# Performance work log

Hardware: AMD Instinct MI355X
Metric: run time of the kernel (lower is better)

## Reference

```python
import jax, jax.numpy as jnp
import numpy as np

HEADS = 16
DIM_HEAD = 64
RMS_EPS = 1.1920929e-07  # torch.finfo(float32).eps (torch RMSNorm eps=None default)
ROPE_THETA = 10000.0


def _rope(x):
    # x: [b, h, n, d]; rotary-embedding-torch style interleaved rotation
    n, d = x.shape[-2], x.shape[-1]
    inv_freq = 1.0 / (ROPE_THETA ** (jnp.arange(0, d, 2, dtype=jnp.float32) / d))
    t = jnp.arange(n, dtype=jnp.float32)
    freqs = t[:, None] * inv_freq[None, :]              # [n, d/2]
    cos = jnp.repeat(jnp.cos(freqs), 2, axis=-1)        # [n, d] interleaved
    sin = jnp.repeat(jnp.sin(freqs), 2, axis=-1)
    x1 = x[..., ::2]
    x2 = x[..., 1::2]
    rot = jnp.stack((-x2, x1), axis=-1).reshape(x.shape)  # rotate_half, interleaved pairs
    return x * cos + rot * sin


def setup_inputs() -> dict:
    key = jax.random.key(0)
    ks = jax.random.split(key, 6)
    b, n, dim = 2, 2048, 1024
    tokens = jax.random.normal(ks[0], (b, n, dim), dtype=jnp.float32)
    norm_weight = jnp.ones((dim,), dtype=jnp.float32)
    wq = jax.random.normal(ks[1], (dim, dim), dtype=jnp.float32) * 0.02
    wk = jax.random.normal(ks[2], (dim, dim), dtype=jnp.float32) * 0.02
    wv = jax.random.normal(ks[3], (dim, dim), dtype=jnp.float32) * 0.02
    wo = jax.random.normal(ks[4], (dim, dim), dtype=jnp.float32) * 0.02
    return {"tokens": tokens, "norm_weight": norm_weight, "wq": wq, "wk": wk, "wv": wv, "wo": wo}


def reference(tokens, norm_weight, wq, wk, wv, wo):
    b, n, dim = tokens.shape
    # RMSNorm (elementwise affine)
    x = tokens * jax.lax.rsqrt(jnp.mean(tokens * tokens, axis=-1, keepdims=True) + RMS_EPS)
    x = x * norm_weight
    # QKV projections (torch Linear: x @ W.T), split heads: b n (h d) -> b h n d
    def split(y):
        return y.reshape(b, n, HEADS, DIM_HEAD).transpose(0, 2, 1, 3)
    q = split(x @ wq.T) * (DIM_HEAD ** -0.5)
    k = split(x @ wk.T)
    v = split(x @ wv.T)
    # rotary embedding (no kv cache -> same positions for q and k)
    q = _rope(q)
    k = _rope(k)
    sim = jnp.einsum('bhid,bhjd->bhij', q, k)
    causal = jnp.triu(jnp.ones((n, n), dtype=bool), k=1)
    sim = jnp.where(causal, -jnp.finfo(sim.dtype).max, sim)
    attn = jax.nn.softmax(sim, axis=-1)
    out = jnp.einsum('bhij,bhjd->bhid', attn, v)
    out = out.transpose(0, 2, 1, 3).reshape(b, n, dim)  # merge heads
    return out @ wo.T
```

## Files before the change

### kernel.cpp

```cpp
#include <hip/hip_runtime.h>

typedef __bf16 bf16x8 __attribute__((ext_vector_type(8)));
typedef float f32x4 __attribute__((ext_vector_type(4)));

#define DIM 1024
#define NSEQ 2048

#define GL2LDS(g, l) __builtin_amdgcn_global_load_lds( \
    (const __attribute__((address_space(1))) void*)(g), \
    (__attribute__((address_space(3))) void*)(l), 16, 0, 0)

#define MFMA16(a, b, c) __builtin_amdgcn_mfma_f32_16x16x32_bf16(a, b, c, 0, 0, 0)

__global__ __launch_bounds__(256) void pre_kernel(const float* __restrict__ wq,
                                                  const float* __restrict__ wk,
                                                  const float* __restrict__ wv,
                                                  __bf16* __restrict__ dq,
                                                  __bf16* __restrict__ dk,
                                                  __bf16* __restrict__ dv,
                                                  float2* __restrict__ tbl,
                                                  int* __restrict__ counters,
                                                  const float* __restrict__ x,
                                                  const float* __restrict__ g,
                                                  __bf16* __restrict__ xo) {
    int bid = blockIdx.x;
    int t = threadIdx.x;
    if (bid == 0 && t < 8) counters[t] = 0;
    if (bid < 3072) {
        int slice = bid >> 10;
        const float* s = slice == 0 ? wq : (slice == 1 ? wk : wv);
        __bf16*      d = slice == 0 ? dq : (slice == 1 ? dk : dv);
        int i = ((bid & 1023) * 256 + t) * 4;
        float4 f = *(const float4*)(s + i);
        union { uint2 u; __bf16 h[4]; } p;
        p.h[0] = (__bf16)f.x; p.h[1] = (__bf16)f.y;
        p.h[2] = (__bf16)f.z; p.h[3] = (__bf16)f.w;
        *(uint2*)(d + i) = p.u;
    } else if (bid < 3328) {
        int e = (bid - 3072) * 256 + t;
        int pos = e >> 5, dp = e & 31;
        float inv = __expf(-(float)dp * (9.210340371976184f / 32.0f));
        float sn, cs;
        sincosf((float)pos * inv, &sn, &cs);
        tbl[e] = make_float2(cs, sn);
    } else {
        int row = bid - 3328;
        float4 xv = ((const float4*)(x + (size_t)row * DIM))[t];
        float ss = xv.x*xv.x + xv.y*xv.y + xv.z*xv.z + xv.w*xv.w;
        #pragma unroll
        for (int off = 32; off; off >>= 1) ss += __shfl_xor(ss, off, 64);
        __shared__ float red[4];
        if ((t & 63) == 0) red[t >> 6] = ss;
        __syncthreads();
        ss = red[0] + red[1] + red[2] + red[3];
        float r = rsqrtf(ss * (1.0f / 1024.0f) + 1.1920929e-07f);
        float4 gv = ((const float4*)g)[t];
        union { uint2 u; __bf16 h[4]; } p;
        p.h[0] = (__bf16)(xv.x * r * gv.x);
        p.h[1] = (__bf16)(xv.y * r * gv.y);
        p.h[2] = (__bf16)(xv.z * r * gv.z);
        p.h[3] = (__bf16)(xv.w * r * gv.w);
        *(uint2*)(xo + (size_t)row * DIM + t * 4) = p.u;
    }
}

template <typename CT, bool ROPE>
__device__ __forceinline__ void gemm_body(const __bf16* __restrict__ A,
                                          const __bf16* __restrict__ B,
                                          CT* __restrict__ C,
                                          int mb, int nb, int ldc, float scale,
                                          __bf16* As, __bf16* Bs,
                                          const float2* __restrict__ tbl) {
    int t = threadIdx.x;
    int w = t >> 6, l = t & 63;
    int wm = (w >> 1) * 64, wn = (w & 1) * 64;
    int lrow = l & 15, lq = l >> 4;
    int sw = lrow & 7;
    f32x4 acc[4][4] = {};

    int srow = w * 32 + (l >> 3);
    int sc8 = ((l & 7) ^ ((l >> 3) & 7)) * 8;
    const __bf16* gA = A + (size_t)(mb * 128 + srow) * 1024 + sc8;
    const __bf16* gB = B + (size_t)(nb * 128 + srow) * 1024 + sc8;
    __bf16* lA = As + (size_t)(w * 32) * 64;
    __bf16* lB = Bs + (size_t)(w * 32) * 64;

    for (int kt = 0; kt < 16; ++kt) {
        int k0 = kt * 64;
        #pragma unroll
        for (int c = 0; c < 4; ++c) {
            GL2LDS(gA + (size_t)c * 8 * 1024 + k0, lA + c * 8 * 64);
            GL2LDS(gB + (size_t)c * 8 * 1024 + k0, lB + c * 8 * 64);
        }
        __syncthreads();
        #pragma unroll
        for (int ch = 0; ch < 2; ++ch) {
            bf16x8 af[4], bfr[4];
            #pragma unroll
            for (int i = 0; i < 4; ++i)
                af[i] = *(const bf16x8*)&As[(wm + i * 16 + lrow) * 64 + ((ch * 4 + lq) ^ sw) * 8];
            #pragma unroll
            for (int i = 0; i < 4; ++i)
                bfr[i] = *(const bf16x8*)&Bs[(wn + i * 16 + lrow) * 64 + ((ch * 4 + lq) ^ sw) * 8];
            #pragma unroll
            for (int rt = 0; rt < 4; ++rt)
                #pragma unroll
                for (int ct = 0; ct < 4; ++ct)
                    acc[rt][ct] = MFMA16(af[rt], bfr[ct], acc[rt][ct]);
        }
        __syncthreads();
    }
    #pragma unroll
    for (int rt = 0; rt < 4; ++rt)
        #pragma unroll
        for (int ct = 0; ct < 4; ++ct) {
            int colg = nb * 128 + wn + ct * 16 + lrow;
            int dp = ((ct * 16 + lrow) & 63) >> 1;
            #pragma unroll
            for (int r = 0; r < 4; ++r) {
                int rowg = mb * 128 + wm + rt * 16 + lq * 4 + r;
                float v = acc[rt][ct][r] * scale;
                if constexpr (ROPE) {
                    float p = __shfl_xor(v, 1, 64);
                    float2 cs = tbl[((rowg & (NSEQ - 1)) << 5) + dp];
                    v = (lrow & 1) ? (v * cs.x + p * cs.y)
                                   : (v * cs.x - p * cs.y);
                }
                C[(size_t)rowg * ldc + colg] = (CT)v;
            }
        }
}

__global__ __launch_bounds__(256) void qkv_kernel(const __bf16* __restrict__ x,
                                                  const __bf16* __restrict__ wq,
                                                  const __bf16* __restrict__ wk,
                                                  const __bf16* __restrict__ wv,
                                                  __bf16* __restrict__ qb,
                                                  __bf16* __restrict__ kb,
                                                  __bf16* __restrict__ vtb,
                                                  const float2* __restrict__ tbl) {
    __shared__ __bf16 As[128 * 64];
    __shared__ __bf16 Bs[128 * 64];
    int bm = blockIdx.x, bn = blockIdx.y, z = blockIdx.z;
    if (z == 0)      gemm_body<__bf16, true >(x,  wq, qb,  bm, bn, 1024,
                                       0.125f * 1.44269504088896340736f, As, Bs, tbl);
    else if (z == 1) gemm_body<__bf16, true >(x,  wk, kb,  bm, bn, 1024, 1.0f, As, Bs, tbl);
    else             gemm_body<__bf16, false>(wv, x,  vtb, bn, bm, 4096, 1.0f, As, Bs, tbl);
}

__global__ __launch_bounds__(256) void wo_kernel(const __bf16* __restrict__ A,
                                                 const float* __restrict__ B,
                                                 float* __restrict__ C) {
    __shared__ __bf16 As[128 * 64];
    __shared__ __bf16 Bs[64 * 64];
    int mb = blockIdx.x, nb = blockIdx.y;
    int t = threadIdx.x;
    int w = t >> 6, l = t & 63;
    int wm = (w >> 1) * 64, wn = (w & 1) * 32;
    int lrow = l & 15, lq = l >> 4;
    int sw = lrow & 7;
    f32x4 acc[4][2] = {};

    int srowA = w * 32 + (l >> 3);
    int sc8 = ((l & 7) ^ ((l >> 3) & 7)) * 8;
    const __bf16* gA = A + (size_t)(mb * 128 + srowA) * 1024 + sc8;
    __bf16* lA = As + (size_t)(w * 32) * 64;

    int rB = t >> 2;
    const float* gB = B + (size_t)(nb * 64 + rB) * 1024 + (t & 3) * 16;
    int db0 = (rB * 8 + (((t & 3) * 2    ) ^ (rB & 7))) * 8;
    int db1 = (rB * 8 + (((t & 3) * 2 + 1) ^ (rB & 7))) * 8;

    for (int kt = 0; kt < 16; ++kt) {
        int k0 = kt * 64;
        #pragma unroll
        for (int c = 0; c < 4; ++c)
            GL2LDS(gA + (size_t)c * 8 * 1024 + k0, lA + c * 8 * 64);
        float4 b0 = *(const float4*)(gB + k0);
        float4 b1 = *(const float4*)(gB + k0 + 4);
        float4 b2 = *(const float4*)(gB + k0 + 8);
        float4 b3 = *(const float4*)(gB + k0 + 12);
        union { uint4 u; __bf16 h[8]; } p0, p1;
        p0.h[0] = (__bf16)b0.x; p0.h[1] = (__bf16)b0.y;
        p0.h[2] = (__bf16)b0.z; p0.h[3] = (__bf16)b0.w;
        p0.h[4] = (__bf16)b1.x; p0.h[5] = (__bf16)b1.y;
        p0.h[6] = (__bf16)b1.z; p0.h[7] = (__bf16)b1.w;
        p1.h[0] = (__bf16)b2.x; p1.h[1] = (__bf16)b2.y;
        p1.h[2] = (__bf16)b2.z; p1.h[3] = (__bf16)b2.w;
        p1.h[4] = (__bf16)b3.x; p1.h[5] = (__bf16)b3.y;
        p1.h[6] = (__bf16)b3.z; p1.h[7] = (__bf16)b3.w;
        *(uint4*)&Bs[db0] = p0.u;
        *(uint4*)&Bs[db1] = p1.u;
        __syncthreads();
        #pragma unroll
        for (int ch = 0; ch < 2; ++ch) {
            bf16x8 af[4], bfr[2];
            #pragma unroll
            for (int i = 0; i < 4; ++i)
                af[i] = *(const bf16x8*)&As[(wm + i * 16 + lrow) * 64 + ((ch * 4 + lq) ^ sw) * 8];
            #pragma unroll
            for (int i = 0; i < 2; ++i)
                bfr[i] = *(const bf16x8*)&Bs[(wn + i * 16 + lrow) * 64 + ((ch * 4 + lq) ^ sw) * 8];
            #pragma unroll
            for (int rt = 0; rt < 4; ++rt)
                #pragma unroll
                for (int ct = 0; ct < 2; ++ct)
                    acc[rt][ct] = MFMA16(af[rt], bfr[ct], acc[rt][ct]);
        }
        __syncthreads();
    }
    #pragma unroll
    for (int rt = 0; rt < 4; ++rt)
        #pragma unroll
        for (int ct = 0; ct < 2; ++ct)
            #pragma unroll
            for (int r = 0; r < 4; ++r) {
                int row = mb * 128 + wm + rt * 16 + lq * 4 + r;
                int col = nb * 64 + wn + ct * 16 + lrow;
                C[(size_t)row * 1024 + col] = acc[rt][ct][r];
            }
}

__global__ __launch_bounds__(256, 3) void attn_kernel(const __bf16* __restrict__ q,
                                                      const __bf16* __restrict__ kk,
                                                      const __bf16* __restrict__ vt,
                                                      __bf16* __restrict__ o,
                                                      int* __restrict__ counters) {
    int xcd = blockIdx.x & 7;
    int t = threadIdx.x;
    int w = t >> 6, l = t & 63;
    int lrow = l & 15, lq = l >> 4;
    int rw = (w & 1) * 32;
    int par = w >> 1;
    int row0 = t >> 3;
    int cb = t & 7;

    __shared__ __bf16 Kt[2][64 * 64];
    __shared__ __bf16 Vs[2][64 * 64];
    __shared__ __bf16 Ps[4][32 * 72];
    __shared__ int s_item;
    __bf16* pw = Ps[w];

    int dsw0 = (row0 * 8 + (cb ^ (row0 & 7))) * 8;
    int dsw1 = ((row0 + 32) * 8 + (cb ^ (row0 & 7))) * 8;

    if (t == 0) s_item = atomicAdd(&counters[xcd], 1);
    __syncthreads();
    int item = s_item;
    bool pf_valid = false;
    uint4 k0a, k0b, v0a, v0b, k1a, k1b, v1a, v1b;

    while (item < 128) {
        int iq = 31 - (item >> 2);
        int bh = xcd * 4 + (item & 3);
        int h = bh & 15;
        int b = bh >> 4;
        int rowbase = b * NSEQ;

        const __bf16* kbase = kk + (size_t)rowbase * DIM + h * 64;
        const __bf16* vbase = vt + (size_t)(h * 64) * 4096 + b * 2048;
        const __bf16* kg = kbase + (size_t)row0 * DIM + cb * 8;
        const __bf16* vg = vbase + (size_t)row0 * 4096 + cb * 8;

        bf16x8 qf[2][2];
        #pragma unroll
        for (int g = 0; g < 2; ++g) {
            const __bf16* qp = q + (size_t)(rowbase + iq * 64 + rw + g * 16 + lrow) * DIM + h * 64;
            qf[g][0] = *(const bf16x8*)(qp + lq * 8);
            qf[g][1] = *(const bf16x8*)(qp + 32 + lq * 8);
        }

        f32x4 oacc[2][4] = {};
        float m_r[2] = {-1e30f, -1e30f};
        float l_r[2] = {0.0f, 0.0f};

        if (!pf_valid) {
            k0a = *(const uint4*)(kg);
            k0b = *(const uint4*)(kg + (size_t)32 * DIM);
            v0a = *(const uint4*)(vg);
            v0b = *(const uint4*)(vg + (size_t)32 * 4096);
            if (iq >= 1) {
                k1a = *(const uint4*)(kg + (size_t)64 * DIM);
                k1b = *(const uint4*)(kg + (size_t)96 * DIM);
                v1a = *(const uint4*)(vg + 64);
                v1b = *(const uint4*)(vg + (size_t)32 * 4096 + 64);
            }
        }
        *(uint4*)&Kt[0][dsw0] = k0a; *(uint4*)&Kt[0][dsw1] = k0b;
        *(uint4*)&Vs[0][dsw0] = v0a; *(uint4*)&Vs[0][dsw1] = v0b;
        if (iq >= 1) {
            *(uint4*)&Kt[1][dsw0] = k1a; *(uint4*)&Kt[1][dsw1] = k1b;
            *(uint4*)&Vs[1][dsw0] = v1a; *(uint4*)&Vs[1][dsw1] = v1b;
        }
        __syncthreads();

        int R = (iq + 2) >> 1;
        for (int rd = 0; rd < R; ++rd) {
            if (rd == R - 1 && t == 0)
                s_item = atomicAdd(&counters[xcd], 1);
            int jt = 2 * rd + par;
            bool pf = (rd + 1 < R);
            if (pf) {
                int je = 2 * rd + 2;
                size_t ko = (size_t)je * 64 * DIM;
                k0a = *(const uint4*)(kg + ko);
                k0b = *(const uint4*)(kg + ko + (size_t)32 * DIM);
                v0a = *(const uint4*)(vg + je * 64);
                v0b = *(const uint4*)(vg + (size_t)32 * 4096 + je * 64);
                if (je + 1 <= iq) {
                    k1a = *(const uint4*)(kg + ko + (size_t)64 * DIM);
                    k1b = *(const uint4*)(kg + ko + (size_t)96 * DIM);
                    v1a = *(const uint4*)(vg + je * 64 + 64);
                    v1b = *(const uint4*)(vg + (size_t)32 * 4096 + je * 64 + 64);
                }
            }
            if (jt <= iq) {
                const __bf16* Kb = Kt[par];
                const __bf16* Vb = Vs[par];
                int sw = lrow & 7;
                f32x4 st[2][4];
                __builtin_amdgcn_s_setprio(1);
                #pragma unroll
                for (int ct = 0; ct < 4; ++ct) {
                    int rr = (ct * 16 + lrow) * 8;
                    bf16x8 ka0 = *(const bf16x8*)&Kb[(rr + (lq ^ sw)) * 8];
                    bf16x8 ka1 = *(const bf16x8*)&Kb[(rr + ((4 + lq) ^ sw)) * 8];
                    #pragma unroll
                    for (int g = 0; g < 2; ++g) {
                        f32x4 z = {};
                        z = MFMA16(ka0, qf[g][0], z);
                        z = MFMA16(ka1, qf[g][1], z);
                        st[g][ct] = z;
                    }
                }
                __builtin_amdgcn_s_setprio(0);
                if (jt == iq) {
                    #pragma unroll
                    for (int g = 0; g < 2; ++g) {
                        int qrel = rw + g * 16 + lrow;
                        #pragma unroll
                        for (int ct = 0; ct < 4; ++ct)
                            #pragma unroll
                            for (int r = 0; r < 4; ++r)
                                if (ct * 16 + lq * 4 + r > qrel) st[g][ct][r] = -3.0e38f;
                    }
                }
                #pragma unroll
                for (int g = 0; g < 2; ++g) {
                    float m0 = fmaxf(fmaxf(st[g][0][0], st[g][0][1]), fmaxf(st[g][0][2], st[g][0][3]));
                    float m1 = fmaxf(fmaxf(st[g][1][0], st[g][1][1]), fmaxf(st[g][1][2], st[g][1][3]));
                    float m2 = fmaxf(fmaxf(st[g][2][0], st[g][2][1]), fmaxf(st[g][2][2], st[g][2][3]));
                    float m3 = fmaxf(fmaxf(st[g][3][0], st[g][3][1]), fmaxf(st[g][3][2], st[g][3][3]));
                    float mx = fmaxf(fmaxf(m0, m1), fmaxf(m2, m3));
                    mx = fmaxf(mx, __shfl_xor(mx, 16, 64));
                    mx = fmaxf(mx, __shfl_xor(mx, 32, 64));
                    if (!__all(mx - m_r[g] <= 8.0f)) {
                        float mnew = fmaxf(m_r[g], mx);
                        float alpha = __builtin_amdgcn_exp2f(m_r[g] - mnew);
                        l_r[g] *= alpha;
                        #pragma unroll
                        for (int ct = 0; ct < 4; ++ct)
                            #pragma unroll
                            for (int r = 0; r < 4; ++r) oacc[g][ct][r] *= alpha;
                        m_r[g] = mnew;
                    }
                    float ps = 0.0f;
                    #pragma unroll
                    for (int ct = 0; ct < 4; ++ct)
                        #pragma unroll
                        for (int r = 0; r < 4; ++r) {
                            float p = __builtin_amdgcn_exp2f(st[g][ct][r] - m_r[g]);
                            st[g][ct][r] = p;
                            ps += p;
                        }
                    ps += __shfl_xor(ps, 16, 64);
                    ps += __shfl_xor(ps, 32, 64);
                    l_r[g] += ps;
                }
                #pragma unroll
                for (int g = 0; g < 2; ++g)
                    #pragma unroll
                    for (int ct = 0; ct < 4; ++ct) {
                        union { uint2 u; __bf16 h4[4]; } pk;
                        #pragma unroll
                        for (int r = 0; r < 4; ++r) pk.h4[r] = (__bf16)st[g][ct][r];
                        *(uint2*)&pw[(g * 16 + lrow) * 72 + ct * 16 + lq * 4] = pk.u;
                    }
                bf16x8 pb[2][2];
                #pragma unroll
                for (int g = 0; g < 2; ++g) {
                    pb[g][0] = *(const bf16x8*)&pw[(g * 16 + lrow) * 72 + lq * 8];
                    pb[g][1] = *(const bf16x8*)&pw[(g * 16 + lrow) * 72 + 32 + lq * 8];
                }
                __builtin_amdgcn_s_setprio(1);
                #pragma unroll
                for (int ct = 0; ct < 4; ++ct) {
                    int rr = (ct * 16 + lrow) * 8;
                    bf16x8 va0 = *(const bf16x8*)&Vb[(rr + (lq ^ sw)) * 8];
                    bf16x8 va1 = *(const bf16x8*)&Vb[(rr + ((4 + lq) ^ sw)) * 8];
                    #pragma unroll
                    for (int g = 0; g < 2; ++g) {
                        oacc[g][ct] = MFMA16(va0, pb[g][0], oacc[g][ct]);
                        oacc[g][ct] = MFMA16(va1, pb[g][1], oacc[g][ct]);
                    }
                }
                __builtin_amdgcn_s_setprio(0);
            }
            if (pf) {
                __syncthreads();
                *(uint4*)&Kt[0][dsw0] = k0a; *(uint4*)&Kt[0][dsw1] = k0b;
                *(uint4*)&Vs[0][dsw0] = v0a; *(uint4*)&Vs[0][dsw1] = v0b;
                if (2 * rd + 3 <= iq) {
                    *(uint4*)&Kt[1][dsw0] = k1a; *(uint4*)&Kt[1][dsw1] = k1b;
                    *(uint4*)&Vs[1][dsw0] = v1a; *(uint4*)&Vs[1][dsw1] = v1b;
                }
                __syncthreads();
            }
        }

        __syncthreads();
        int nitem = s_item;
        if (nitem < 128) {
            int niq = 31 - (nitem >> 2);
            int nbh = xcd * 4 + (nitem & 3);
            int nh = nbh & 15;
            int nb_ = nbh >> 4;
            const __bf16* nkg = kk + ((size_t)(nb_ * NSEQ) + row0) * DIM + nh * 64 + cb * 8;
            const __bf16* nvg = vt + (size_t)(nh * 64 + row0) * 4096 + nb_ * 2048 + cb * 8;
            k0a = *(const uint4*)(nkg);
            k0b = *(const uint4*)(nkg + (size_t)32 * DIM);
            v0a = *(const uint4*)(nvg);
            v0b = *(const uint4*)(nvg + (size_t)32 * 4096);
            if (niq >= 1) {
                k1a = *(const uint4*)(nkg + (size_t)64 * DIM);
                k1b = *(const uint4*)(nkg + (size_t)96 * DIM);
                v1a = *(const uint4*)(nvg + 64);
                v1b = *(const uint4*)(nvg + (size_t)32 * 4096 + 64);
            }
        }
        float* sc = (float*)&Ps[0][0];
        float* base = sc + (w & 1) * 2304 + l * 36;
        if (par == 1) {
            #pragma unroll
            for (int g = 0; g < 2; ++g)
                #pragma unroll
                for (int ct = 0; ct < 4; ++ct)
                    *(f32x4*)(base + g * 16 + ct * 4) = oacc[g][ct];
            base[32] = m_r[0]; base[33] = m_r[1];
            base[34] = l_r[0]; base[35] = l_r[1];
        }
        __syncthreads();
        if (par == 0) {
            #pragma unroll
            for (int g = 0; g < 2; ++g) {
                float mb = base[32 + g], lb = base[34 + g];
                float m = fmaxf(m_r[g], mb);
                float a  = __builtin_amdgcn_exp2f(m_r[g] - m);
                float bb = __builtin_amdgcn_exp2f(mb - m);
                float rcp = 1.0f / (a * l_r[g] + bb * lb);
                const size_t orow = (size_t)(rowbase + iq * 64 + rw + g * 16 + lrow) * DIM + h * 64;
                #pragma unroll
                for (int ct = 0; ct < 4; ++ct) {
                    f32x4 ob = *(const f32x4*)(base + g * 16 + ct * 4);
                    union { uint2 u; __bf16 h4[4]; } pk;
                    #pragma unroll
                    for (int r = 0; r < 4; ++r)
                        pk.h4[r] = (__bf16)((a * oacc[g][ct][r] + bb * ob[r]) * rcp);
                    *(uint2*)(o + orow + ct * 16 + lq * 4) = pk.u;
                }
            }
        }
        item = nitem;
        pf_valid = true;
    }
}

extern "C" void kernel_launch(void* const* d_in, const int* in_sizes, int n_in,
                              void* d_out, int out_size, void* d_ws, size_t ws_size,
                              hipStream_t stream) {
    const float* tokens = (const float*)d_in[0];
    const float* gamma  = (const float*)d_in[1];
    const float* wq = (const float*)d_in[2];
    const float* wk = (const float*)d_in[3];
    const float* wv = (const float*)d_in[4];
    const float* wo = (const float*)d_in[5];

    __bf16* ws  = (__bf16*)d_ws;
    __bf16* x   = ws;
    __bf16* qb  = x   + (size_t)4096 * 1024;
    __bf16* kb  = qb  + (size_t)4096 * 1024;
    __bf16* vtb = kb  + (size_t)4096 * 1024;
    __bf16* ao  = x;
    float*  out = (float*)d_out;

    __bf16* wqb = (__bf16*)d_out;
    __bf16* wkb = wqb + (size_t)1024 * 1024;
    __bf16* wvb = wkb + (size_t)1024 * 1024;
    float2* tbl = (float2*)((char*)d_out + (size_t)6 * 1024 * 1024);
    int* counters = (int*)((char*)d_out + (size_t)8 * 1024 * 1024);

    pre_kernel<<<7424, 256, 0, stream>>>(wq, wk, wv, wqb, wkb, wvb, tbl, counters,
                                         tokens, gamma, x);

    qkv_kernel<<<dim3(32, 8, 3), 256, 0, stream>>>(x, wqb, wkb, wvb, qb, kb, vtb, tbl);

    attn_kernel<<<768, 256, 0, stream>>>(qb, kb, vtb, ao, counters);

    wo_kernel<<<dim3(32, 16), 256, 0, stream>>>(ao, wo, out);
}
```

Baseline: 202.0 us.

## Double-buffer QKV GEMM LDS tiles with K=32 stages to overlap loads

The QKV projection GEMM now uses two LDS buffers of 128x32 per operand instead of one 128x64 tile. The next K-slice is issued with global_load_lds while the current slice is consumed by MFMAs, leaving one barrier per step instead of two. The LDS swizzle is reworked for the 32-wide rows. The iteration count doubles, so there are more barriers overall, and LDS footprint per block is unchanged.

```diff
diff --git a/kernel.cpp b/kernel.cpp
--- a/kernel.cpp
+++ b/kernel.cpp
@@ -69,47 +69,54 @@
                                           const __bf16* __restrict__ B,
                                           CT* __restrict__ C,
                                           int mb, int nb, int ldc, float scale,
-                                          __bf16* As, __bf16* Bs,
+                                          __bf16* As0, __bf16* As1,
+                                          __bf16* Bs0, __bf16* Bs1,
                                           const float2* __restrict__ tbl) {
     int t = threadIdx.x;
     int w = t >> 6, l = t & 63;
     int wm = (w >> 1) * 64, wn = (w & 1) * 64;
     int lrow = l & 15, lq = l >> 4;
-    int sw = lrow & 7;
+    int cbr = (lq ^ (lrow & 3) ^ ((lrow >> 2) & 3)) * 8;
     f32x4 acc[4][4] = {};
 
-    int srow = w * 32 + (l >> 3);
-    int sc8 = ((l & 7) ^ ((l >> 3) & 7)) * 8;
-    const __bf16* gA = A + (size_t)(mb * 128 + srow) * 1024 + sc8;
-    const __bf16* gB = B + (size_t)(nb * 128 + srow) * 1024 + sc8;
-    __bf16* lA = As + (size_t)(w * 32) * 64;
-    __bf16* lB = Bs + (size_t)(w * 32) * 64;
-
-    for (int kt = 0; kt < 16; ++kt) {
-        int k0 = kt * 64;
-        #pragma unroll
-        for (int c = 0; c < 4; ++c) {
-            GL2LDS(gA + (size_t)c * 8 * 1024 + k0, lA + c * 8 * 64);
-            GL2LDS(gB + (size_t)c * 8 * 1024 + k0, lB + c * 8 * 64);
-        }
-        __syncthreads();
-        #pragma unroll
-        for (int ch = 0; ch < 2; ++ch) {
-            bf16x8 af[4], bfr[4];
-            #pragma unroll
-            for (int i = 0; i < 4; ++i)
-                af[i] = *(const bf16x8*)&As[(wm + i * 16 + lrow) * 64 + ((ch * 4 + lq) ^ sw) * 8];
-            #pragma unroll
-            for (int i = 0; i < 4; ++i)
-                bfr[i] = *(const bf16x8*)&Bs[(wn + i * 16 + lrow) * 64 + ((ch * 4 + lq) ^ sw) * 8];
-            #pragma unroll
-            for (int rt = 0; rt < 4; ++rt)
-                #pragma unroll
-                for (int ct = 0; ct < 4; ++ct)
-                    acc[rt][ct] = MFMA16(af[rt], bfr[ct], acc[rt][ct]);
-        }
-        __syncthreads();
+    int srow = w * 16 + (l >> 2);
+    int scb = ((l & 3) ^ ((l >> 2) & 3) ^ (l >> 4)) * 8;
+    const __bf16* gA = A + (size_t)(mb * 128 + srow) * 1024 + scb;
+    const __bf16* gB = B + (size_t)(nb * 128 + srow) * 1024 + scb;
+    int lbase = (w * 16) * 32;
+
+    auto stage = [&](int kt, __bf16* dA, __bf16* dB) {
+        #pragma unroll
+        for (int c = 0; c < 2; ++c) {
+            GL2LDS(gA + (size_t)c * 64 * 1024 + kt * 32, dA + lbase + c * 64 * 32);
+            GL2LDS(gB + (size_t)c * 64 * 1024 + kt * 32, dB + lbase + c * 64 * 32);
+        }
+    };
+    auto step = [&](int kt, const __bf16* rA, const __bf16* rB,
+                    __bf16* sA, __bf16* sB) {
+        if (kt + 1 < 32) stage(kt + 1, sA, sB);
+        bf16x8 af[4], bfr[4];
+        #pragma unroll
+        for (int i = 0; i < 4; ++i)
+            af[i] = *(const bf16x8*)&rA[(wm + i * 16 + lrow) * 32 + cbr];
+        #pragma unroll
+        for (int i = 0; i < 4; ++i)
+            bfr[i] = *(const bf16x8*)&rB[(wn + i * 16 + lrow) * 32 + cbr];
+        #pragma unroll
+        for (int rt = 0; rt < 4; ++rt)
+            #pragma unroll
+            for (int ct = 0; ct < 4; ++ct)
+                acc[rt][ct] = MFMA16(af[rt], bfr[ct], acc[rt][ct]);
+        __syncthreads();
+    };
+
+    stage(0, As0, Bs0);
+    __syncthreads();
+    for (int kt = 0; kt < 32; kt += 2) {
+        step(kt,     As0, Bs0, As1, Bs1);
+        step(kt + 1, As1, Bs1, As0, Bs0);
     }
+
     #pragma unroll
     for (int rt = 0; rt < 4; ++rt)
         #pragma unroll
@@ -139,13 +146,16 @@
                                                   __bf16* __restrict__ kb,
                                                   __bf16* __restrict__ vtb,
                                                   const float2* __restrict__ tbl) {
-    __shared__ __bf16 As[128 * 64];
-    __shared__ __bf16 Bs[128 * 64];
+    __shared__ __bf16 As[2][128 * 32];
+    __shared__ __bf16 Bs[2][128 * 32];
     int bm = blockIdx.x, bn = blockIdx.y, z = blockIdx.z;
     if (z == 0)      gemm_body<__bf16, true >(x,  wq, qb,  bm, bn, 1024,
-                                       0.125f * 1.44269504088896340736f, As, Bs, tbl);
-    else if (z == 1) gemm_body<__bf16, true >(x,  wk, kb,  bm, bn, 1024, 1.0f, As, Bs, tbl);
-    else             gemm_body<__bf16, false>(wv, x,  vtb, bn, bm, 4096, 1.0f, As, Bs, tbl);
+                                       0.125f * 1.44269504088896340736f,
+                                       As[0], As[1], Bs[0], Bs[1], tbl);
+    else if (z == 1) gemm_body<__bf16, true >(x,  wk, kb,  bm, bn, 1024, 1.0f,
+                                       As[0], As[1], Bs[0], Bs[1], tbl);
+    else             gemm_body<__bf16, false>(wv, x,  vtb, bn, bm, 4096, 1.0f,
+                                       As[0], As[1], Bs[0], Bs[1], tbl);
 }
 
 __global__ __launch_bounds__(256) void wo_kernel(const __bf16* __restrict__ A,
```

After: 206.6 us. +2.2%, slower.

## Fuse all four stages into one persistent cooperative kernel with grid syncs

Applied to the files above, without the earlier changes.

Replaces the four separate launches (pre, qkv, attention, output projection) with a single persistent cooperative kernel. Blocks loop over virtual block ids and a grid-wide sync separates the stages, so the per-launch gaps go away. The attention stage also drops its cross-item prefetch of the next work item's K/V tiles and now fetches the item counter at the top of each loop. In exchange, the persistent grid caps occupancy at 3 blocks per CU, the grid syncs have their own cost, and every stage is forced onto the same shared-memory and register budget.

```diff
diff --git a/kernel.cpp b/kernel.cpp
--- a/kernel.cpp
+++ b/kernel.cpp
@@ -1,4 +1,7 @@
 #include <hip/hip_runtime.h>
+#include <hip/hip_cooperative_groups.h>
+
+namespace cg = cooperative_groups;
 
 typedef __bf16 bf16x8 __attribute__((ext_vector_type(8)));
 typedef float f32x4 __attribute__((ext_vector_type(4)));
@@ -12,55 +15,61 @@
 
 #define MFMA16(a, b, c) __builtin_amdgcn_mfma_f32_16x16x32_bf16(a, b, c, 0, 0, 0)
 
-__global__ __launch_bounds__(256) void pre_kernel(const float* __restrict__ wq,
-                                                  const float* __restrict__ wk,
-                                                  const float* __restrict__ wv,
-                                                  __bf16* __restrict__ dq,
-                                                  __bf16* __restrict__ dk,
-                                                  __bf16* __restrict__ dv,
-                                                  float2* __restrict__ tbl,
-                                                  int* __restrict__ counters,
-                                                  const float* __restrict__ x,
-                                                  const float* __restrict__ g,
-                                                  __bf16* __restrict__ xo) {
-    int bid = blockIdx.x;
+#define SMEM_BYTES 51712
+
+__device__ __forceinline__ void pre_stage(int bid, int gdim,
+                                          const float* __restrict__ wq,
+                                          const float* __restrict__ wk,
+                                          const float* __restrict__ wv,
+                                          __bf16* __restrict__ dq,
+                                          __bf16* __restrict__ dk,
+                                          __bf16* __restrict__ dv,
+                                          float2* __restrict__ tbl,
+                                          int* __restrict__ counters,
+                                          const float* __restrict__ x,
+                                          const float* __restrict__ g,
+                                          __bf16* __restrict__ xo,
+                                          char* smem) {
     int t = threadIdx.x;
-    if (bid == 0 && t < 8) counters[t] = 0;
-    if (bid < 3072) {
-        int slice = bid >> 10;
-        const float* s = slice == 0 ? wq : (slice == 1 ? wk : wv);
-        __bf16*      d = slice == 0 ? dq : (slice == 1 ? dk : dv);
-        int i = ((bid & 1023) * 256 + t) * 4;
-        float4 f = *(const float4*)(s + i);
-        union { uint2 u; __bf16 h[4]; } p;
-        p.h[0] = (__bf16)f.x; p.h[1] = (__bf16)f.y;
-        p.h[2] = (__bf16)f.z; p.h[3] = (__bf16)f.w;
-        *(uint2*)(d + i) = p.u;
-    } else if (bid < 3328) {
-        int e = (bid - 3072) * 256 + t;
-        int pos = e >> 5, dp = e & 31;
-        float inv = __expf(-(float)dp * (9.210340371976184f / 32.0f));
-        float sn, cs;
-        sincosf((float)pos * inv, &sn, &cs);
-        tbl[e] = make_float2(cs, sn);
-    } else {
-        int row = bid - 3328;
-        float4 xv = ((const float4*)(x + (size_t)row * DIM))[t];
-        float ss = xv.x*xv.x + xv.y*xv.y + xv.z*xv.z + xv.w*xv.w;
-        #pragma unroll
-        for (int off = 32; off; off >>= 1) ss += __shfl_xor(ss, off, 64);
-        __shared__ float red[4];
-        if ((t & 63) == 0) red[t >> 6] = ss;
-        __syncthreads();
-        ss = red[0] + red[1] + red[2] + red[3];
-        float r = rsqrtf(ss * (1.0f / 1024.0f) + 1.1920929e-07f);
-        float4 gv = ((const float4*)g)[t];
-        union { uint2 u; __bf16 h[4]; } p;
-        p.h[0] = (__bf16)(xv.x * r * gv.x);
-        p.h[1] = (__bf16)(xv.y * r * gv.y);
-        p.h[2] = (__bf16)(xv.z * r * gv.z);
-        p.h[3] = (__bf16)(xv.w * r * gv.w);
-        *(uint2*)(xo + (size_t)row * DIM + t * 4) = p.u;
+    float* red = (float*)smem;
+    for (int vb = bid; vb < 7424; vb += gdim) {
+        if (vb == 0 && t < 8) counters[t] = 0;
+        if (vb < 3072) {
+            int slice = vb >> 10;
+            const float* s = slice == 0 ? wq : (slice == 1 ? wk : wv);
+            __bf16*      d = slice == 0 ? dq : (slice == 1 ? dk : dv);
+            int i = ((vb & 1023) * 256 + t) * 4;
+            float4 f = *(const float4*)(s + i);
+            union { uint2 u; __bf16 h[4]; } p;
+            p.h[0] = (__bf16)f.x; p.h[1] = (__bf16)f.y;
+            p.h[2] = (__bf16)f.z; p.h[3] = (__bf16)f.w;
+            *(uint2*)(d + i) = p.u;
+        } else if (vb < 3328) {
+            int e = (vb - 3072) * 256 + t;
+            int pos = e >> 5, dp = e & 31;
+            float inv = __expf(-(float)dp * (9.210340371976184f / 32.0f));
+            float sn, cs;
+            sincosf((float)pos * inv, &sn, &cs);
+            tbl[e] = make_float2(cs, sn);
+        } else {
+            int row = vb - 3328;
+            float4 xv = ((const float4*)(x + (size_t)row * DIM))[t];
+            float ss = xv.x*xv.x + xv.y*xv.y + xv.z*xv.z + xv.w*xv.w;
+            #pragma unroll
+            for (int off = 32; off; off >>= 1) ss += __shfl_xor(ss, off, 64);
+            if ((t & 63) == 0) red[t >> 6] = ss;
+            __syncthreads();
+            ss = red[0] + red[1] + red[2] + red[3];
+            float r = rsqrtf(ss * (1.0f / 1024.0f) + 1.1920929e-07f);
+            float4 gv = ((const float4*)g)[t];
+            union { uint2 u; __bf16 h[4]; } p;
+            p.h[0] = (__bf16)(xv.x * r * gv.x);
+            p.h[1] = (__bf16)(xv.y * r * gv.y);
+            p.h[2] = (__bf16)(xv.z * r * gv.z);
+            p.h[3] = (__bf16)(xv.w * r * gv.w);
+            *(uint2*)(xo + (size_t)row * DIM + t * 4) = p.u;
+            __syncthreads();
+        }
     }
 }
 
@@ -131,102 +140,36 @@
         }
 }
 
-__global__ __launch_bounds__(256) void qkv_kernel(const __bf16* __restrict__ x,
-                                                  const __bf16* __restrict__ wq,
-                                                  const __bf16* __restrict__ wk,
-                                                  const __bf16* __restrict__ wv,
-                                                  __bf16* __restrict__ qb,
-                                                  __bf16* __restrict__ kb,
-                                                  __bf16* __restrict__ vtb,
-                                                  const float2* __restrict__ tbl) {
-    __shared__ __bf16 As[128 * 64];
-    __shared__ __bf16 Bs[128 * 64];
-    int bm = blockIdx.x, bn = blockIdx.y, z = blockIdx.z;
-    if (z == 0)      gemm_body<__bf16, true >(x,  wq, qb,  bm, bn, 1024,
-                                       0.125f * 1.44269504088896340736f, As, Bs, tbl);
-    else if (z == 1) gemm_body<__bf16, true >(x,  wk, kb,  bm, bn, 1024, 1.0f, As, Bs, tbl);
-    else             gemm_body<__bf16, false>(wv, x,  vtb, bn, bm, 4096, 1.0f, As, Bs, tbl);
-}
-
-__global__ __launch_bounds__(256) void wo_kernel(const __bf16* __restrict__ A,
-                                                 const float* __restrict__ B,
-                                                 float* __restrict__ C) {
-    __shared__ __bf16 As[128 * 64];
-    __shared__ __bf16 Bs[64 * 64];
-    int mb = blockIdx.x, nb = blockIdx.y;
-    int t = threadIdx.x;
-    int w = t >> 6, l = t & 63;
-    int wm = (w >> 1) * 64, wn = (w & 1) * 32;
-    int lrow = l & 15, lq = l >> 4;
-    int sw = lrow & 7;
-    f32x4 acc[4][2] = {};
-
-    int srowA = w * 32 + (l >> 3);
-    int sc8 = ((l & 7) ^ ((l >> 3) & 7)) * 8;
-    const __bf16* gA = A + (size_t)(mb * 128 + srowA) * 1024 + sc8;
-    __bf16* lA = As + (size_t)(w * 32) * 64;
-
-    int rB = t >> 2;
-    const float* gB = B + (size_t)(nb * 64 + rB) * 1024 + (t & 3) * 16;
-    int db0 = (rB * 8 + (((t & 3) * 2    ) ^ (rB & 7))) * 8;
-    int db1 = (rB * 8 + (((t & 3) * 2 + 1) ^ (rB & 7))) * 8;
-
-    for (int kt = 0; kt < 16; ++kt) {
-        int k0 = kt * 64;
-        #pragma unroll
-        for (int c = 0; c < 4; ++c)
-            GL2LDS(gA + (size_t)c * 8 * 1024 + k0, lA + c * 8 * 64);
-        float4 b0 = *(const float4*)(gB + k0);
-        float4 b1 = *(const float4*)(gB + k0 + 4);
-        float4 b2 = *(const float4*)(gB + k0 + 8);
-        float4 b3 = *(const float4*)(gB + k0 + 12);
-        union { uint4 u; __bf16 h[8]; } p0, p1;
-        p0.h[0] = (__bf16)b0.x; p0.h[1] = (__bf16)b0.y;
-        p0.h[2] = (__bf16)b0.z; p0.h[3] = (__bf16)b0.w;
-        p0.h[4] = (__bf16)b1.x; p0.h[5] = (__bf16)b1.y;
-        p0.h[6] = (__bf16)b1.z; p0.h[7] = (__bf16)b1.w;
-        p1.h[0] = (__bf16)b2.x; p1.h[1] = (__bf16)b2.y;
-        p1.h[2] = (__bf16)b2.z; p1.h[3] = (__bf16)b2.w;
-        p1.h[4] = (__bf16)b3.x; p1.h[5] = (__bf16)b3.y;
-        p1.h[6] = (__bf16)b3.z; p1.h[7] = (__bf16)b3.w;
-        *(uint4*)&Bs[db0] = p0.u;
-        *(uint4*)&Bs[db1] = p1.u;
-        __syncthreads();
-        #pragma unroll
-        for (int ch = 0; ch < 2; ++ch) {
-            bf16x8 af[4], bfr[2];
-            #pragma unroll
-            for (int i = 0; i < 4; ++i)
-                af[i] = *(const bf16x8*)&As[(wm + i * 16 + lrow) * 64 + ((ch * 4 + lq) ^ sw) * 8];
-            #pragma unroll
-            for (int i = 0; i < 2; ++i)
-                bfr[i] = *(const bf16x8*)&Bs[(wn + i * 16 + lrow) * 64 + ((ch * 4 + lq) ^ sw) * 8];
-            #pragma unroll
-            for (int rt = 0; rt < 4; ++rt)
-                #pragma unroll
-                for (int ct = 0; ct < 2; ++ct)
-                    acc[rt][ct] = MFMA16(af[rt], bfr[ct], acc[rt][ct]);
-        }
-        __syncthreads();
+__device__ __forceinline__ void qkv_stage(int bid, int gdim,
+                                          const __bf16* __restrict__ x,
+                                          const __bf16* __restrict__ wqb,
+                                          const __bf16* __restrict__ wkb,
+                                          const __bf16* __restrict__ wvb,
+                                          __bf16* __restrict__ qb,
+                                          __bf16* __restrict__ kb,
+                                          __bf16* __restrict__ vtb,
+                                          const float2* __restrict__ tbl,
+                                          char* smem) {
+    __bf16* As = (__bf16*)smem;
+    __bf16* Bs = As + 8192;
+    for (int vb = bid; vb < 768; vb += gdim) {
+        int z = vb >> 8, rem = vb & 255;
+        int bn = rem >> 5, bm = rem & 31;
+        if (z == 0)      gemm_body<__bf16, true >(x,   wqb, qb,  bm, bn, 1024,
+                                           0.125f * 1.44269504088896340736f, As, Bs, tbl);
+        else if (z == 1) gemm_body<__bf16, true >(x,   wkb, kb,  bm, bn, 1024, 1.0f, As, Bs, tbl);
+        else             gemm_body<__bf16, false>(wvb, x,   vtb, bn, bm, 4096, 1.0f, As, Bs, tbl);
     }
-    #pragma unroll
-    for (int rt = 0; rt < 4; ++rt)
-        #pragma unroll
-        for (int ct = 0; ct < 2; ++ct)
-            #pragma unroll
-            for (int r = 0; r < 4; ++r) {
-                int row = mb * 128 + wm + rt * 16 + lq * 4 + r;
-                int col = nb * 64 + wn + ct * 16 + lrow;
-                C[(size_t)row * 1024 + col] = acc[rt][ct][r];
-            }
-}
-
-__global__ __launch_bounds__(256, 3) void attn_kernel(const __bf16* __restrict__ q,
-                                                      const __bf16* __restrict__ kk,
-                                                      const __bf16* __restrict__ vt,
-                                                      __bf16* __restrict__ o,
-                                                      int* __restrict__ counters) {
-    int xcd = blockIdx.x & 7;
+}
+
+__device__ __forceinline__ void attn_stage(int bid,
+                                           const __bf16* __restrict__ q,
+                                           const __bf16* __restrict__ kk,
+                                           const __bf16* __restrict__ vt,
+                                           __bf16* __restrict__ o,
+                                           int* __restrict__ counters,
+                                           char* smem) {
+    int xcd = bid & 7;
     int t = threadIdx.x;
     int w = t >> 6, l = t & 63;
     int lrow = l & 15, lq = l >> 4;
@@ -235,22 +178,19 @@
     int row0 = t >> 3;
     int cb = t & 7;
 
-    __shared__ __bf16 Kt[2][64 * 64];
-    __shared__ __bf16 Vs[2][64 * 64];
-    __shared__ __bf16 Ps[4][32 * 72];
-    __shared__ int s_item;
-    __bf16* pw = Ps[w];
-
-    int dsw0 = (row0 * 8 + (cb ^ (row0 & 7))) * 8;
-    int dsw1 = ((row0 + 32) * 8 + (cb ^ (row0 & 7))) * 8;
-
-    if (t == 0) s_item = atomicAdd(&counters[xcd], 1);
-    __syncthreads();
-    int item = s_item;
-    bool pf_valid = false;
-    uint4 k0a, k0b, v0a, v0b, k1a, k1b, v1a, v1b;
-
-    while (item < 128) {
+    __bf16* Kt0 = (__bf16*)smem;
+    __bf16* Kt1 = Kt0 + 4096;
+    __bf16* Vs0 = Kt1 + 4096;
+    __bf16* Vs1 = Vs0 + 4096;
+    __bf16* Ps  = Vs1 + 4096;
+    int* s_item = (int*)(smem + 51200);
+    __bf16* pw = Ps + w * 2304;
+
+    for (;;) {
+        if (t == 0) *s_item = atomicAdd(&counters[xcd], 1);
+        __syncthreads();
+        int item = *s_item;
+        if (item >= 128) break;
         int iq = 31 - (item >> 2);
         int bh = xcd * 4 + (item & 3);
         int h = bh & 15;
@@ -259,8 +199,6 @@
 
         const __bf16* kbase = kk + (size_t)rowbase * DIM + h * 64;
         const __bf16* vbase = vt + (size_t)(h * 64) * 4096 + b * 2048;
-        const __bf16* kg = kbase + (size_t)row0 * DIM + cb * 8;
-        const __bf16* vg = vbase + (size_t)row0 * 4096 + cb * 8;
 
         bf16x8 qf[2][2];
         #pragma unroll
@@ -274,30 +212,32 @@
         float m_r[2] = {-1e30f, -1e30f};
         float l_r[2] = {0.0f, 0.0f};
 
-        if (!pf_valid) {
-            k0a = *(const uint4*)(kg);
-            k0b = *(const uint4*)(kg + (size_t)32 * DIM);
-            v0a = *(const uint4*)(vg);
-            v0b = *(const uint4*)(vg + (size_t)32 * 4096);
-            if (iq >= 1) {
-                k1a = *(const uint4*)(kg + (size_t)64 * DIM);
-                k1b = *(const uint4*)(kg + (size_t)96 * DIM);
-                v1a = *(const uint4*)(vg + 64);
-                v1b = *(const uint4*)(vg + (size_t)32 * 4096 + 64);
-            }
-        }
-        *(uint4*)&Kt[0][dsw0] = k0a; *(uint4*)&Kt[0][dsw1] = k0b;
-        *(uint4*)&Vs[0][dsw0] = v0a; *(uint4*)&Vs[0][dsw1] = v0b;
+        const __bf16* kg = kbase + (size_t)row0 * DIM + cb * 8;
+        const __bf16* vg = vbase + (size_t)row0 * 4096 + cb * 8;
+        int dsw0 = (row0 * 8 + (cb ^ (row0 & 7))) * 8;
+        int dsw1 = ((row0 + 32) * 8 + (cb ^ (row0 & 7))) * 8;
+
+        uint4 k0a, k0b, v0a, v0b, k1a, k1b, v1a, v1b;
+        k0a = *(const uint4*)(kg);
+        k0b = *(const uint4*)(kg + (size_t)32 * DIM);
+        v0a = *(const uint4*)(vg);
+        v0b = *(const uint4*)(vg + (size_t)32 * 4096);
         if (iq >= 1) {
-            *(uint4*)&Kt[1][dsw0] = k1a; *(uint4*)&Kt[1][dsw1] = k1b;
-            *(uint4*)&Vs[1][dsw0] = v1a; *(uint4*)&Vs[1][dsw1] = v1b;
+            k1a = *(const uint4*)(kg + (size_t)64 * DIM);
+            k1b = *(const uint4*)(kg + (size_t)96 * DIM);
+            v1a = *(const uint4*)(vg + 64);
+            v1b = *(const uint4*)(vg + (size_t)32 * 4096 + 64);
+        }
+        *(uint4*)&Kt0[dsw0] = k0a; *(uint4*)&Kt0[dsw1] = k0b;
+        *(uint4*)&Vs0[dsw0] = v0a; *(uint4*)&Vs0[dsw1] = v0b;
+        if (iq >= 1) {
+            *(uint4*)&Kt1[dsw0] = k1a; *(uint4*)&Kt1[dsw1] = k1b;
+            *(uint4*)&Vs1[dsw0] = v1a; *(uint4*)&Vs1[dsw1] = v1b;
         }
         __syncthreads();
 
         int R = (iq + 2) >> 1;
         for (int rd = 0; rd < R; ++rd) {
-            if (rd == R - 1 && t == 0)
-                s_item = atomicAdd(&counters[xcd], 1);
             int jt = 2 * rd + par;
             bool pf = (rd + 1 < R);
             if (pf) {
@@ -315,8 +255,8 @@
                 }
             }
             if (jt <= iq) {
-                const __bf16* Kb = Kt[par];
-                const __bf16* Vb = Vs[par];
+                const __bf16* Kb = par ? Kt1 : Kt0;
+                const __bf16* Vb = par ? Vs1 : Vs0;
                 int sw = lrow & 7;
                 f32x4 st[2][4];
                 __builtin_amdgcn_s_setprio(1);
@@ -408,37 +348,18 @@
             }
             if (pf) {
                 __syncthreads();
-                *(uint4*)&Kt[0][dsw0] = k0a; *(uint4*)&Kt[0][dsw1] = k0b;
-                *(uint4*)&Vs[0][dsw0] = v0a; *(uint4*)&Vs[0][dsw1] = v0b;
+                *(uint4*)&Kt0[dsw0] = k0a; *(uint4*)&Kt0[dsw1] = k0b;
+                *(uint4*)&Vs0[dsw0] = v0a; *(uint4*)&Vs0[dsw1] = v0b;
                 if (2 * rd + 3 <= iq) {
-                    *(uint4*)&Kt[1][dsw0] = k1a; *(uint4*)&Kt[1][dsw1] = k1b;
-                    *(uint4*)&Vs[1][dsw0] = v1a; *(uint4*)&Vs[1][dsw1] = v1b;
+                    *(uint4*)&Kt1[dsw0] = k1a; *(uint4*)&Kt1[dsw1] = k1b;
+                    *(uint4*)&Vs1[dsw0] = v1a; *(uint4*)&Vs1[dsw1] = v1b;
                 }
                 __syncthreads();
             }
         }
 
         __syncthreads();
-        int nitem = s_item;
-        if (nitem < 128) {
-            int niq = 31 - (nitem >> 2);
-            int nbh = xcd * 4 + (nitem & 3);
-            int nh = nbh & 15;
-            int nb_ = nbh >> 4;
-            const __bf16* nkg = kk + ((size_t)(nb_ * NSEQ) + row0) * DIM + nh * 64 + cb * 8;
-            const __bf16* nvg = vt + (size_t)(nh * 64 + row0) * 4096 + nb_ * 2048 + cb * 8;
-            k0a = *(const uint4*)(nkg);
-            k0b = *(const uint4*)(nkg + (size_t)32 * DIM);
-            v0a = *(const uint4*)(nvg);
-            v0b = *(const uint4*)(nvg + (size_t)32 * 4096);
-            if (niq >= 1) {
-                k1a = *(const uint4*)(nkg + (size_t)64 * DIM);
-                k1b = *(const uint4*)(nkg + (size_t)96 * DIM);
-                v1a = *(const uint4*)(nvg + 64);
-                v1b = *(const uint4*)(nvg + (size_t)32 * 4096 + 64);
-            }
-        }
-        float* sc = (float*)&Ps[0][0];
+        float* sc = (float*)Ps;
         float* base = sc + (w & 1) * 2304 + l * 36;
         if (par == 1) {
             #pragma unroll
@@ -470,9 +391,114 @@
                 }
             }
         }
-        item = nitem;
-        pf_valid = true;
     }
+}
+
+__device__ __forceinline__ void wo_stage(int bid, int gdim,
+                                         const __bf16* __restrict__ A,
+                                         const float* __restrict__ B,
+                                         float* __restrict__ C,
+                                         char* smem) {
+    __bf16* As = (__bf16*)smem;
+    __bf16* Bs = As + 8192;
+    int t = threadIdx.x;
+    int w = t >> 6, l = t & 63;
+    int wm = (w >> 1) * 64, wn = (w & 1) * 32;
+    int lrow = l & 15, lq = l >> 4;
+    int sw = lrow & 7;
+    int srowA = w * 32 + (l >> 3);
+    int sc8 = ((l & 7) ^ ((l >> 3) & 7)) * 8;
+    __bf16* lA = As + (size_t)(w * 32) * 64;
+    int rB = t >> 2;
+    int db0 = (rB * 8 + (((t & 3) * 2    ) ^ (rB & 7))) * 8;
+    int db1 = (rB * 8 + (((t & 3) * 2 + 1) ^ (rB & 7))) * 8;
+
+    for (int vb = bid; vb < 512; vb += gdim) {
+        int mb = vb & 31, nb = vb >> 5;
+        f32x4 acc[4][2] = {};
+        const __bf16* gA = A + (size_t)(mb * 128 + srowA) * 1024 + sc8;
+        const float*  gB = B + (size_t)(nb * 64 + rB) * 1024 + (t & 3) * 16;
+
+        for (int kt = 0; kt < 16; ++kt) {
+            int k0 = kt * 64;
+            #pragma unroll
+            for (int c = 0; c < 4; ++c)
+                GL2LDS(gA + (size_t)c * 8 * 1024 + k0, lA + c * 8 * 64);
+            float4 b0 = *(const float4*)(gB + k0);
+            float4 b1 = *(const float4*)(gB + k0 + 4);
+            float4 b2 = *(const float4*)(gB + k0 + 8);
+            float4 b3 = *(const float4*)(gB + k0 + 12);
+            union { uint4 u; __bf16 h[8]; } p0, p1;
+            p0.h[0] = (__bf16)b0.x; p0.h[1] = (__bf16)b0.y;
+            p0.h[2] = (__bf16)b0.z; p0.h[3] = (__bf16)b0.w;
+            p0.h[4] = (__bf16)b1.x; p0.h[5] = (__bf16)b1.y;
+            p0.h[6] = (__bf16)b1.z; p0.h[7] = (__bf16)b1.w;
+            p1.h[0] = (__bf16)b2.x; p1.h[1] = (__bf16)b2.y;
+            p1.h[2] = (__bf16)b2.z; p1.h[3] = (__bf16)b2.w;
+            p1.h[4] = (__bf16)b3.x; p1.h[5] = (__bf16)b3.y;
+            p1.h[6] = (__bf16)b3.z; p1.h[7] = (__bf16)b3.w;
+            *(uint4*)&Bs[db0] = p0.u;
+            *(uint4*)&Bs[db1] = p1.u;
+            __syncthreads();
+            #pragma unroll
+            for (int ch = 0; ch < 2; ++ch) {
+                bf16x8 af[4], bfr[2];
+                #pragma unroll
+                for (int i = 0; i < 4; ++i)
+                    af[i] = *(const bf16x8*)&As[(wm + i * 16 + lrow) * 64 + ((ch * 4 + lq) ^ sw) * 8];
+                #pragma unroll
+                for (int i = 0; i < 2; ++i)
+                    bfr[i] = *(const bf16x8*)&Bs[(wn + i * 16 + lrow) * 64 + ((ch * 4 + lq) ^ sw) * 8];
+                #pragma unroll
+                for (int rt = 0; rt < 4; ++rt)
+                    #pragma unroll
+                    for (int ct = 0; ct < 2; ++ct)
+                        acc[rt][ct] = MFMA16(af[rt], bfr[ct], acc[rt][ct]);
+            }
+            __syncthreads();
+        }
+        #pragma unroll
+        for (int rt = 0; rt < 4; ++rt)
+            #pragma unroll
+            for (int ct = 0; ct < 2; ++ct)
+                #pragma unroll
+                for (int r = 0; r < 4; ++r) {
+                    int row = mb * 128 + wm + rt * 16 + lq * 4 + r;
+                    int col = nb * 64 + wn + ct * 16 + lrow;
+                    C[(size_t)row * 1024 + col] = acc[rt][ct][r];
+                }
+    }
+}
+
+__global__ __launch_bounds__(256, 3) void mega_kernel(
+        const float* __restrict__ wq, const float* __restrict__ wk,
+        const float* __restrict__ wv,
+        __bf16* __restrict__ wqb, __bf16* __restrict__ wkb,
+        __bf16* __restrict__ wvb,
+        float2* __restrict__ tbl, int* __restrict__ counters,
+        const float* __restrict__ tokens, const float* __restrict__ gamma,
+        __bf16* __restrict__ x, __bf16* __restrict__ qb,
+        __bf16* __restrict__ kb, __bf16* __restrict__ vtb,
+        const float* __restrict__ woW, float* __restrict__ out) {
+    extern __shared__ char smem[];
+    cg::grid_group grid = cg::this_grid();
+    int bid = blockIdx.x;
+    int gdim = gridDim.x;
+
+    pre_stage(bid, gdim, wq, wk, wv, wqb, wkb, wvb, tbl, counters,
+              tokens, gamma, x, smem);
+    __threadfence();
+    grid.sync();
+
+    qkv_stage(bid, gdim, x, wqb, wkb, wvb, qb, kb, vtb, tbl, smem);
+    __threadfence();
+    grid.sync();
+
+    attn_stage(bid, qb, kb, vtb, x, counters, smem);
+    __threadfence();
+    grid.sync();
+
+    wo_stage(bid, gdim, x, woW, out, smem);
 }
 
 extern "C" void kernel_launch(void* const* d_in, const int* in_sizes, int n_in,
@@ -490,7 +516,6 @@
     __bf16* qb  = x   + (size_t)4096 * 1024;
     __bf16* kb  = qb  + (size_t)4096 * 1024;
     __bf16* vtb = kb  + (size_t)4096 * 1024;
-    __bf16* ao  = x;
     float*  out = (float*)d_out;
 
     __bf16* wqb = (__bf16*)d_out;
@@ -499,12 +524,20 @@
     float2* tbl = (float2*)((char*)d_out + (size_t)6 * 1024 * 1024);
     int* counters = (int*)((char*)d_out + (size_t)8 * 1024 * 1024);
 
-    pre_kernel<<<7424, 256, 0, stream>>>(wq, wk, wv, wqb, wkb, wvb, tbl, counters,
-                                         tokens, gamma, x);
-
-    qkv_kernel<<<dim3(32, 8, 3), 256, 0, stream>>>(x, wqb, wkb, wvb, qb, kb, vtb, tbl);
-
-    attn_kernel<<<768, 256, 0, stream>>>(qb, kb, vtb, ao, counters);
-
-    wo_kernel<<<dim3(32, 16), 256, 0, stream>>>(ao, wo, out);
-}
+    int maxb = 0;
+    hipError_t qerr = hipOccupancyMaxActiveBlocksPerMultiprocessor(
+        &maxb, (const void*)mega_kernel, 256, (size_t)SMEM_BYTES);
+    int blocks_per_cu = (qerr == hipSuccess && maxb >= 1) ? (maxb > 3 ? 3 : maxb) : 2;
+    int grid = 256 * blocks_per_cu;
+
+    void* args[] = {
+        (void*)&wq, (void*)&wk, (void*)&wv,
+        (void*)&wqb, (void*)&wkb, (void*)&wvb,
+        (void*)&tbl, (void*)&counters,
+        (void*)&tokens, (void*)&gamma,
+        (void*)&x, (void*)&qb, (void*)&kb, (void*)&vtb,
+        (void*)&wo, (void*)&out
+    };
+    hipLaunchCooperativeKernel((const void*)mega_kernel, dim3(grid), dim3(256),
+                               args, SMEM_BYTES, stream);
+}
```

Measured after the change: 433.9 us. +114.8%, slower.
